# Kernel optimization log

Measured on AMD Instinct MI355X. Metric: run time of the kernel, lower is better.

Reference implementation:

```python
import jax, jax.numpy as jnp
import numpy as np

C_QKV = 1024
C_HIDDEN = 64
NUM_HEADS = 16
INF = 1e9


def setup_inputs() -> dict:
    key = jax.random.key(0)
    ks = jax.random.split(key, 10)
    B, S = 2, 2048
    d = C_QKV
    hd = C_HIDDEN * NUM_HEADS
    sc = 0.02
    return {
        "input_qkv": jax.random.normal(ks[0], (B, S, d), jnp.float32),
        "mask": jnp.ones((B, 1, 1, S), jnp.float32),
        "bias": jax.random.normal(ks[1], (1, NUM_HEADS, S, S), jnp.float32) * sc,
        "wq": jax.random.normal(ks[2], (d, hd), jnp.float32) * sc,
        "wk": jax.random.normal(ks[3], (d, hd), jnp.float32) * sc,
        "wv": jax.random.normal(ks[4], (d, hd), jnp.float32) * sc,
        "wg": jax.random.normal(ks[5], (d, hd), jnp.float32) * sc,
        "bg": jnp.zeros((hd,), jnp.float32),
        "wo": jax.random.normal(ks[6], (hd, d), jnp.float32) * sc,
        "bo": jnp.zeros((d,), jnp.float32),
    }


def reference(input_qkv, mask, bias, wq, wk, wv, wg, bg, wo, bo):
    B, S, _ = input_qkv.shape
    H, C = NUM_HEADS, C_HIDDEN
    # projections -> [B, H, S, C]
    q = (input_qkv @ wq).reshape(B, S, H, C).transpose(0, 2, 1, 3)
    k = (input_qkv @ wk).reshape(B, S, H, C).transpose(0, 2, 1, 3)
    v = (input_qkv @ wv).reshape(B, S, H, C).transpose(0, 2, 1, 3)
    q = q / jnp.asarray(C, q.dtype) ** 0.5
    # scores [B, H, S, S] with additive mask and pair bias
    a = jnp.einsum("bhqc,bhkc->bhqk", q, k)
    a = a + (mask - 1.0) * INF + bias
    a = jax.nn.softmax(a, axis=-1)
    o = jnp.einsum("bhqk,bhkc->bhqc", a, v).transpose(0, 2, 1, 3)  # [B,S,H,C]
    gate = jax.nn.sigmoid(input_qkv @ wg + bg).reshape(B, S, H, C)
    o = (o * gate).reshape(B, S, H * C)
    return o @ wo + bo
```

## Files before the change

### kernel.cpp

```cpp
#include <hip/hip_runtime.h>
#include <hip/hip_bf16.h>
#include <stdint.h>

typedef unsigned short u16;
typedef __attribute__((ext_vector_type(8))) short short8;
typedef __attribute__((ext_vector_type(4))) short short4v;
typedef __attribute__((ext_vector_type(4))) float f32x4;

#define MFMA16 __builtin_amdgcn_mfma_f32_16x16x32_bf16

#define GLOAD_LDS16(gsrc, ldst) \
  __builtin_amdgcn_global_load_lds((const __attribute__((address_space(1))) void*)(gsrc), \
                                   (__attribute__((address_space(3))) void*)(ldst), 16, 0, 0)

__device__ __forceinline__ u16 f2bf(float x) {
  union { float f; uint32_t u; } v; v.f = x;
  uint32_t r = v.u + 0x7FFFu + ((v.u >> 16) & 1u);
  return (u16)(r >> 16);
}
__device__ __forceinline__ u16 f2bf_rn(float x) {
  __hip_bfloat16 h = __float2bfloat16(x);
  return *reinterpret_cast<u16*>(&h);
}
__device__ __forceinline__ float bf2f(u16 b) {
  union { uint32_t u; float f; } v; v.u = ((uint32_t)b) << 16;
  return v.f;
}

__global__ __launch_bounds__(256) void convert_bf16_kernel(
    const float* __restrict__ in, u16* __restrict__ out, int n) {
  int i = (blockIdx.x * 256 + threadIdx.x) * 8;
  if (i >= n) return;
  float4 a = *(const float4*)(in + i);
  float4 b = *(const float4*)(in + i + 4);
  short8 t;
  t[0] = (short)f2bf(a.x); t[1] = (short)f2bf(a.y);
  t[2] = (short)f2bf(a.z); t[3] = (short)f2bf(a.w);
  t[4] = (short)f2bf(b.x); t[5] = (short)f2bf(b.y);
  t[6] = (short)f2bf(b.z); t[7] = (short)f2bf(b.w);
  *(short8*)(out + i) = t;
}

__global__ __launch_bounds__(256) void transpose_w64_4(
    const float* __restrict__ w0, const float* __restrict__ w1,
    const float* __restrict__ w2, const float* __restrict__ w3,
    u16* __restrict__ WT) {
  __shared__ float tile[64][68];
  const int t = threadIdx.x;
  const int z = blockIdx.z;
  const float* W = (z == 0) ? w0 : (z == 1) ? w1 : (z == 2) ? w2 : w3;
  u16* dst_base = WT + (size_t)z * 1024 * 1024;
  const int k0 = blockIdx.x * 64, n0 = blockIdx.y * 64;
  {
    int r = t >> 2, c0 = (t & 3) * 16;
    const float* src = W + (size_t)(k0 + r) * 1024 + n0 + c0;
#pragma unroll
    for (int j = 0; j < 16; j += 4) {
      float4 v = *(const float4*)(src + j);
      tile[r][c0 + j + 0] = v.x; tile[r][c0 + j + 1] = v.y;
      tile[r][c0 + j + 2] = v.z; tile[r][c0 + j + 3] = v.w;
    }
  }
  __syncthreads();
  {
    int n = t >> 2, kq = (t & 3) * 16;
    short8 t0, t1;
#pragma unroll
    for (int j = 0; j < 8; ++j)  t0[j] = (short)f2bf(tile[kq + j][n]);
#pragma unroll
    for (int j = 0; j < 8; ++j)  t1[j] = (short)f2bf(tile[kq + 8 + j][n]);
    u16* dst = dst_base + (size_t)(n0 + n) * 1024 + k0 + kq;
    *(short8*)dst = t0;
    *(short8*)(dst + 8) = t1;
  }
}

__global__ __launch_bounds__(256) void transpose_w64(
    const float* __restrict__ W, u16* __restrict__ WT, int KK, int NN) {
  __shared__ float tile[64][68];
  const int t = threadIdx.x;
  const int k0 = blockIdx.x * 64, n0 = blockIdx.y * 64;
  {
    int r = t >> 2, c0 = (t & 3) * 16;
    const float* src = W + (size_t)(k0 + r) * NN + n0 + c0;
#pragma unroll
    for (int j = 0; j < 16; j += 4) {
      float4 v = *(const float4*)(src + j);
      tile[r][c0 + j + 0] = v.x; tile[r][c0 + j + 1] = v.y;
      tile[r][c0 + j + 2] = v.z; tile[r][c0 + j + 3] = v.w;
    }
  }
  __syncthreads();
  {
    int n = t >> 2, kq = (t & 3) * 16;
    short8 t0, t1;
#pragma unroll
    for (int j = 0; j < 8; ++j)  t0[j] = (short)f2bf(tile[kq + j][n]);
#pragma unroll
    for (int j = 0; j < 8; ++j)  t1[j] = (short)f2bf(tile[kq + 8 + j][n]);
    u16* dst = WT + (size_t)(n0 + n) * KK + k0 + kq;
    *(short8*)dst = t0;
    *(short8*)(dst + 8) = t1;
  }
}

__global__ __launch_bounds__(256) void transpose_v64(
    const u16* __restrict__ vin, u16* __restrict__ vout) {
  __shared__ u16 tile[64][80];
  const int t = threadIdx.x;
  const int s0 = blockIdx.x * 64;
  const int bh = blockIdx.y;
  const int b = bh >> 4, h = bh & 15;
  {
    int r = t >> 2, c0 = (t & 3) * 16;
    const u16* src = vin + (size_t)(b * 2048 + s0 + r) * 1024 + h * 64 + c0;
    *(short8*)&tile[r][c0] = *(const short8*)src;
    *(short8*)&tile[r][c0 + 8] = *(const short8*)(src + 8);
  }
  __syncthreads();
  {
    int c = t >> 2, s4 = (t & 3) * 16;
    short8 t0, t1;
#pragma unroll
    for (int j = 0; j < 8; ++j) t0[j] = (short)tile[s4 + j][c];
#pragma unroll
    for (int j = 0; j < 8; ++j) t1[j] = (short)tile[s4 + 8 + j][c];
    u16* dst = vout + (size_t)(bh * 64 + c) * 2048 + s0 + s4;
    *(short8*)dst = t0;
    *(short8*)(dst + 8) = t1;
  }
}

__global__ __launch_bounds__(256) void gemm_bt128(
    const u16* __restrict__ A, const u16* __restrict__ BTbase,
    void* __restrict__ dstbase, const float* __restrict__ bvec, int mode) {
  const int K = 1024;
  const int tid = threadIdx.x, lane = tid & 63, w = tid >> 6;
  const int wr = w >> 1, wc = w & 1;
  const int l15 = lane & 15, lg = lane >> 4;
  const int z = (mode < 0) ? (int)blockIdx.z : mode;
  const u16* BT = (mode < 0) ? BTbase + (size_t)z * 1024 * 1024 : BTbase;
  const int rbase = blockIdx.x * 128;
  const int nbase = blockIdx.y * 128;
  __shared__ u16 lsA[128 * 64];
  __shared__ u16 lsB[128 * 64];
  f32x4 acc[4][4] = {};
  const int col8 = (lane & 7) * 8;
  for (int kt = 0; kt < K / 64; ++kt) {
#pragma unroll
    for (int i = 0; i < 4; ++i) {
      int row = w * 32 + i * 8 + (lane >> 3);
      const u16* sa = A + (size_t)(rbase + row) * K + kt * 64 + col8;
      GLOAD_LDS16(sa, lsA + (w * 32 + i * 8) * 64 + lane * 8);
      const u16* sb = BT + (size_t)(nbase + row) * K + kt * 64 + col8;
      GLOAD_LDS16(sb, lsB + (w * 32 + i * 8) * 64 + lane * 8);
    }
    __syncthreads();
#pragma unroll
    for (int kk = 0; kk < 2; ++kk) {
      short8 af[4], bfr[4];
#pragma unroll
      for (int m = 0; m < 4; ++m)
        af[m] = *(const short8*)&lsA[(wr * 64 + m * 16 + l15) * 64 + kk * 32 + lg * 8];
#pragma unroll
      for (int n = 0; n < 4; ++n)
        bfr[n] = *(const short8*)&lsB[(wc * 64 + n * 16 + l15) * 64 + kk * 32 + lg * 8];
#pragma unroll
      for (int m = 0; m < 4; ++m)
#pragma unroll
        for (int n = 0; n < 4; ++n)
          acc[m][n] = MFMA16(af[m], bfr[n], acc[m][n], 0, 0, 0);
    }
    __syncthreads();
  }
  const int r0 = rbase + wr * 64;
  const int c0 = nbase + wc * 64;
  if (z == 4) {
    float* out = (float*)dstbase;
#pragma unroll
    for (int m = 0; m < 4; ++m)
#pragma unroll
      for (int n = 0; n < 4; ++n)
#pragma unroll
        for (int i = 0; i < 4; ++i) {
          int r = r0 + m * 16 + lg * 4 + i;
          int c = c0 + n * 16 + l15;
          out[(size_t)r * 1024 + c] = acc[m][n][i] + bvec[c];
        }
  } else {
    u16* dq = (u16*)dstbase + (size_t)z * 4096 * 1024;
#pragma unroll
    for (int m = 0; m < 4; ++m)
#pragma unroll
      for (int n = 0; n < 4; ++n)
#pragma unroll
        for (int i = 0; i < 4; ++i) {
          int r = r0 + m * 16 + lg * 4 + i;
          int c = c0 + n * 16 + l15;
          float v = acc[m][n][i];
          if (z == 0) v *= 0.125f;
          else if (z == 3) v = 1.f / (1.f + __expf(-(v + bvec[c])));
          dq[(size_t)r * 1024 + c] = f2bf(v);
        }
  }
}

__global__ __launch_bounds__(256, 3) void attn_kernel(
    const u16* __restrict__ qws, const u16* __restrict__ kws,
    const u16* __restrict__ vt, const u16* __restrict__ gws,
    const float* __restrict__ bias, const float* __restrict__ mask,
    u16* __restrict__ og) {
  const int tid = threadIdx.x;
  const int lane = tid & 63;
  const int w = tid >> 6;
  const int l15 = lane & 15, lg = lane >> 4;
  const int bx = blockIdx.x;
  const int qt = (bx & 7) | ((bx >> 4) << 3);
  const int b = (bx >> 3) & 1;
  const int h = blockIdx.y;

  __shared__ __align__(16) u16 ring[4][4096];
  __shared__ __align__(16) u16 lsP[4][1280];
  __shared__ __align__(16) u16 lsM[2048];

  const float* bias_base = bias + ((size_t)h * 2048 + qt * 128) * 2048;
  const u16* vt_base = vt + (size_t)((b * 16 + h) * 64) * 2048;
  const u16* k_base = kws + (size_t)(b * 2048) * 1024 + h * 64;

  {
    float4 m0 = *(const float4*)(mask + b * 2048 + tid * 8);
    float4 m1 = *(const float4*)(mask + b * 2048 + tid * 8 + 4);
    short8 mm;
    mm[0] = (short)f2bf((m0.x - 1.f) * 1e9f); mm[1] = (short)f2bf((m0.y - 1.f) * 1e9f);
    mm[2] = (short)f2bf((m0.z - 1.f) * 1e9f); mm[3] = (short)f2bf((m0.w - 1.f) * 1e9f);
    mm[4] = (short)f2bf((m1.x - 1.f) * 1e9f); mm[5] = (short)f2bf((m1.y - 1.f) * 1e9f);
    mm[6] = (short)f2bf((m1.z - 1.f) * 1e9f); mm[7] = (short)f2bf((m1.w - 1.f) * 1e9f);
    *(short8*)&lsM[tid * 8] = mm;
  }

  const size_t qrow0 = (size_t)(b * 2048 + qt * 128 + w * 32 + l15) * 1024 + h * 64;
  const size_t qrow1 = qrow0 + 16 * 1024;
  short8 qf00 = *(const short8*)(qws + qrow0 + lg * 8);
  short8 qf01 = *(const short8*)(qws + qrow0 + 32 + lg * 8);
  short8 qf10 = *(const short8*)(qws + qrow1 + lg * 8);
  short8 qf11 = *(const short8*)(qws + qrow1 + 32 + lg * 8);
  asm volatile("" :: "v"(qf00), "v"(qf01), "v"(qf10), "v"(qf11));
  asm volatile("s_waitcnt vmcnt(0)" ::: "memory");

  f32x4 O[2][4] = {};
  float lacc0 = 0.f, lacc1 = 0.f;
  f32x4 bA0, bA1, bA2, bA3, bB0, bB1, bB2, bB3, bC0, bC1, bC2, bC3;

#define STAGE_KV(SLOT, KW) {                                                        \
    int r_ = tid >> 3, cg_ = tid & 7;                                               \
    GLOAD_LDS16(k_base + (size_t)((KW) * 32 + r_) * 1024 + ((cg_ ^ (r_ & 7)) * 8),  \
                &ring[SLOT][tid * 8]);                                              \
    int c_ = tid >> 2, kg_ = tid & 3;                                               \
    int sw_ = (c_ & 3) ^ ((c_ >> 2) & 3);                                           \
    GLOAD_LDS16(vt_base + (size_t)c_ * 2048 + (KW) * 32 + ((kg_ ^ sw_) * 8),        \
                &ring[SLOT][2048 + tid * 8]); }

#define BIAS_ISSUE(R0, R1, R2, R3, KW) {                                            \
    const float* bp_ = bias_base + (size_t)(w * 32 + l15) * 2048 + (KW) * 32 + lg * 4; \
    asm volatile("global_load_dwordx4 %0, %1, off" : "=v"(R0) : "v"(bp_));          \
    asm volatile("global_load_dwordx4 %0, %1, off" : "=v"(R1) : "v"(bp_ + 16));     \
    asm volatile("global_load_dwordx4 %0, %1, off" : "=v"(R2) : "v"(bp_ + 16 * 2048)); \
    asm volatile("global_load_dwordx4 %0, %1, off" : "=v"(R3) : "v"(bp_ + 16 * 2048 + 16)); \
  }

#define COMPUTE(SLOT, KB, BR00, BR01, BR10, BR11) {                                 \
    const u16* Kc_ = &ring[SLOT][0];                                                \
    const u16* Vc_ = &ring[SLOT][2048];                                             \
    const int sw_ = l15 & 7;                                                        \
    short8 kf0a = *(const short8*)&Kc_[(l15) * 64 + ((lg ^ sw_) * 8)];              \
    short8 kf0b = *(const short8*)&Kc_[(l15) * 64 + (((4 + lg) ^ sw_) * 8)];        \
    short8 kf1a = *(const short8*)&Kc_[(16 + l15) * 64 + ((lg ^ sw_) * 8)];         \
    short8 kf1b = *(const short8*)&Kc_[(16 + l15) * 64 + (((4 + lg) ^ sw_) * 8)];   \
    short4v mk0 = *(const short4v*)&lsM[(KB) * 32 + lg * 4];                        \
    short4v mk1 = *(const short4v*)&lsM[(KB) * 32 + 16 + lg * 4];                   \
    f32x4 ci00, ci01, ci10, ci11;                                                   \
    _Pragma("unroll") for (int i = 0; i < 4; ++i) {                                 \
      float m0_ = bf2f((u16)mk0[i]), m1_ = bf2f((u16)mk1[i]);                       \
      ci00[i] = BR00[i] + m0_; ci01[i] = BR01[i] + m1_;                             \
      ci10[i] = BR10[i] + m0_; ci11[i] = BR11[i] + m1_;                             \
    }                                                                               \
    f32x4 s00 = MFMA16(kf0a, qf00, ci00, 0, 0, 0);                                 \
    s00 = MFMA16(kf0b, qf01, s00, 0, 0, 0);                                         \
    f32x4 s01 = MFMA16(kf1a, qf00, ci01, 0, 0, 0);                                 \
    s01 = MFMA16(kf1b, qf01, s01, 0, 0, 0);                                         \
    f32x4 s10 = MFMA16(kf0a, qf10, ci10, 0, 0, 0);                                 \
    s10 = MFMA16(kf0b, qf11, s10, 0, 0, 0);                                         \
    f32x4 s11 = MFMA16(kf1a, qf10, ci11, 0, 0, 0);                                 \
    s11 = MFMA16(kf1b, qf11, s11, 0, 0, 0);                                         \
    short4v p00, p01, p10, p11;                                                     \
    _Pragma("unroll") for (int i = 0; i < 4; ++i) {                                 \
      float e00 = __expf(s00[i]); lacc0 += e00; p00[i] = (short)f2bf_rn(e00);       \
      float e01 = __expf(s01[i]); lacc0 += e01; p01[i] = (short)f2bf_rn(e01);       \
      float e10 = __expf(s10[i]); lacc1 += e10; p10[i] = (short)f2bf_rn(e10);       \
      float e11 = __expf(s11[i]); lacc1 += e11; p11[i] = (short)f2bf_rn(e11);       \
    }                                                                               \
    *(short4v*)&lsP[w][(l15) * 40 + lg * 4] = p00;                                  \
    *(short4v*)&lsP[w][(l15) * 40 + 16 + lg * 4] = p01;                             \
    *(short4v*)&lsP[w][(16 + l15) * 40 + lg * 4] = p10;                             \
    *(short4v*)&lsP[w][(16 + l15) * 40 + 16 + lg * 4] = p11;                        \
    short8 pf0 = *(const short8*)&lsP[w][(l15) * 40 + lg * 8];                      \
    short8 pf1 = *(const short8*)&lsP[w][(16 + l15) * 40 + lg * 8];                 \
    _Pragma("unroll") for (int cf = 0; cf < 4; ++cf) {                              \
      int c_ = cf * 16 + l15;                                                       \
      short8 vf_ = *(const short8*)&Vc_[c_ * 32 +                                   \
                                        ((lg ^ ((c_ & 3) ^ ((c_ >> 2) & 3))) * 8)]; \
      O[0][cf] = MFMA16(vf_, pf0, O[0][cf], 0, 0, 0);                               \
      O[1][cf] = MFMA16(vf_, pf1, O[1][cf], 0, 0, 0);                               \
    } }

#define BODY(KB, N, X0, X1, X2, X3) {                                               \
    if ((KB) + 3 < 64) STAGE_KV(((KB) + 3) & 3, (KB) + 3);                          \
    COMPUTE((KB) & 3, KB, X0, X1, X2, X3);                                          \
    if ((KB) + 3 < 64) BIAS_ISSUE(X0, X1, X2, X3, (KB) + 3);                        \
    asm volatile("s_waitcnt vmcnt(" #N ")" ::: "memory");                           \
    asm volatile("s_waitcnt lgkmcnt(0)" ::: "memory");                              \
    __builtin_amdgcn_sched_barrier(0);                                              \
    __builtin_amdgcn_s_barrier(); }

  STAGE_KV(0, 0);
  BIAS_ISSUE(bA0, bA1, bA2, bA3, 0);
  STAGE_KV(1, 1);
  BIAS_ISSUE(bB0, bB1, bB2, bB3, 1);
  STAGE_KV(2, 2);
  BIAS_ISSUE(bC0, bC1, bC2, bC3, 2);
  asm volatile("s_waitcnt vmcnt(12)" ::: "memory");
  asm volatile("s_waitcnt lgkmcnt(0)" ::: "memory");
  __builtin_amdgcn_sched_barrier(0);
  __builtin_amdgcn_s_barrier();

  for (int kb3 = 0; kb3 < 60; kb3 += 3) {
    BODY(kb3,     12, bA0, bA1, bA2, bA3);
    BODY(kb3 + 1, 12, bB0, bB1, bB2, bB3);
    BODY(kb3 + 2, 12, bC0, bC1, bC2, bC3);
  }
  BODY(60, 12, bA0, bA1, bA2, bA3);
  BODY(61,  6, bB0, bB1, bB2, bB3);
  BODY(62,  0, bC0, bC1, bC2, bC3);
  BODY(63,  0, bA0, bA1, bA2, bA3);

  lacc0 += __shfl_xor(lacc0, 16); lacc0 += __shfl_xor(lacc0, 32);
  lacc1 += __shfl_xor(lacc1, 16); lacc1 += __shfl_xor(lacc1, 32);
  {
    float inv0 = 1.f / lacc0, inv1 = 1.f / lacc1;
#pragma unroll
    for (int cf = 0; cf < 4; ++cf) {
      short4v ga = *(const short4v*)(gws + qrow0 + cf * 16 + lg * 4);
      short4v gb = *(const short4v*)(gws + qrow1 + cf * 16 + lg * 4);
      short4v oa, ob;
#pragma unroll
      for (int i = 0; i < 4; ++i) {
        oa[i] = (short)f2bf_rn(O[0][cf][i] * inv0 * bf2f((u16)ga[i]));
        ob[i] = (short)f2bf_rn(O[1][cf][i] * inv1 * bf2f((u16)gb[i]));
      }
      *(short4v*)(og + qrow0 + cf * 16 + lg * 4) = oa;
      *(short4v*)(og + qrow1 + cf * 16 + lg * 4) = ob;
    }
  }
#undef STAGE_KV
#undef BIAS_ISSUE
#undef COMPUTE
#undef BODY
}

extern "C" void kernel_launch(void* const* d_in, const int* in_sizes, int n_in,
                              void* d_out, int out_size, void* d_ws, size_t ws_size,
                              hipStream_t stream) {
  const float* x    = (const float*)d_in[0];
  const float* mask = (const float*)d_in[1];
  const float* bias = (const float*)d_in[2];
  const float* wq   = (const float*)d_in[3];
  const float* wk   = (const float*)d_in[4];
  const float* wv   = (const float*)d_in[5];
  const float* wg   = (const float*)d_in[6];
  const float* bg   = (const float*)d_in[7];
  const float* wo   = (const float*)d_in[8];
  const float* bo   = (const float*)d_in[9];
  float* out = (float*)d_out;

  char* ws = (char*)d_ws;
  const size_t MB = 1ull << 20;
  u16* xb   = (u16*)(ws + 0);
  u16* wt   = (u16*)(ws + 8 * MB);
  u16* wot  = (u16*)(ws + 16 * MB);
  u16* proj = (u16*)(ws + 18 * MB);
  u16* vtp  = (u16*)(ws + 50 * MB);
  u16* og   = (u16*)(ws + 58 * MB);
  const size_t PSZ = (size_t)4096 * 1024;

  convert_bf16_kernel<<<2048, 256, 0, stream>>>(x, xb, 4096 * 1024);

  transpose_w64_4<<<dim3(16, 16, 4), 256, 0, stream>>>(wq, wk, wv, wg, wt);
  transpose_w64<<<dim3(16, 16), 256, 0, stream>>>(wo, wot, 1024, 1024);

  gemm_bt128<<<dim3(32, 8, 4), 256, 0, stream>>>(xb, wt, (void*)proj, bg, -1);

  transpose_v64<<<dim3(32, 32), 256, 0, stream>>>(proj + 2 * PSZ, vtp);

  attn_kernel<<<dim3(32, 16), 256, 0, stream>>>(proj, proj + PSZ, vtp, proj + 3 * PSZ,
                                                bias, mask, og);

  gemm_bt128<<<dim3(32, 8, 1), 256, 0, stream>>>(og, wot, (void*)out, bo, 4);
}
```

Baseline: 224.5 us.

## Widen attention key tile to 64 with three-slot ring and fewer barriers

The attention kernel now processes 64 keys per iteration instead of 32. It uses a three-slot K/V ring in LDS, fetches more bias loads per step with a two-step prefetch depth, and switches V to the same XOR swizzle as K. Halving the iteration count cuts the per-step barrier and waitcnt overhead and gives the MFMAs more work between syncs. In exchange, register and LDS use grow, launch bounds drop to 2 blocks per CU, and prefetch depth shrinks from three tiles to two.

```diff
diff --git a/kernel.cpp b/kernel.cpp
--- a/kernel.cpp
+++ b/kernel.cpp
@@ -205,7 +205,7 @@
   }
 }
 
-__global__ __launch_bounds__(256, 3) void attn_kernel(
+__global__ __launch_bounds__(256, 2) void attn_kernel(
     const u16* __restrict__ qws, const u16* __restrict__ kws,
     const u16* __restrict__ vt, const u16* __restrict__ gws,
     const float* __restrict__ bias, const float* __restrict__ mask,
@@ -219,8 +219,8 @@
   const int b = (bx >> 3) & 1;
   const int h = blockIdx.y;
 
-  __shared__ __align__(16) u16 ring[4][4096];
-  __shared__ __align__(16) u16 lsP[4][1280];
+  __shared__ __align__(16) u16 ring[3][8192];
+  __shared__ __align__(16) u16 lsP[4][2304];
   __shared__ __align__(16) u16 lsM[2048];
 
   const float* bias_base = bias + ((size_t)h * 2048 + qt * 128) * 2048;
@@ -249,99 +249,102 @@
 
   f32x4 O[2][4] = {};
   float lacc0 = 0.f, lacc1 = 0.f;
-  f32x4 bA0, bA1, bA2, bA3, bB0, bB1, bB2, bB3, bC0, bC1, bC2, bC3;
+  f32x4 bA0, bA1, bA2, bA3, bA4, bA5, bA6, bA7;
+  f32x4 bB0, bB1, bB2, bB3, bB4, bB5, bB6, bB7;
 
 #define STAGE_KV(SLOT, KW) {                                                        \
-    int r_ = tid >> 3, cg_ = tid & 7;                                               \
-    GLOAD_LDS16(k_base + (size_t)((KW) * 32 + r_) * 1024 + ((cg_ ^ (r_ & 7)) * 8),  \
-                &ring[SLOT][tid * 8]);                                              \
-    int c_ = tid >> 2, kg_ = tid & 3;                                               \
-    int sw_ = (c_ & 3) ^ ((c_ >> 2) & 3);                                           \
-    GLOAD_LDS16(vt_base + (size_t)c_ * 2048 + (KW) * 32 + ((kg_ ^ sw_) * 8),        \
-                &ring[SLOT][2048 + tid * 8]); }
-
-#define BIAS_ISSUE(R0, R1, R2, R3, KW) {                                            \
-    const float* bp_ = bias_base + (size_t)(w * 32 + l15) * 2048 + (KW) * 32 + lg * 4; \
+    _Pragma("unroll") for (int it = 0; it < 2; ++it) {                              \
+      int g_ = it * 256 + tid;                                                      \
+      int r_ = g_ >> 3, cg_ = g_ & 7;                                               \
+      GLOAD_LDS16(k_base + (size_t)((KW) * 64 + r_) * 1024 + ((cg_ ^ (r_ & 7)) * 8),\
+                  &ring[SLOT][g_ * 8]);                                             \
+      GLOAD_LDS16(vt_base + (size_t)r_ * 2048 + (KW) * 64 + ((cg_ ^ (r_ & 7)) * 8), \
+                  &ring[SLOT][4096 + g_ * 8]);                                      \
+    } }
+
+#define BIAS_ISSUE(R0, R1, R2, R3, R4, R5, R6, R7, KW) {                            \
+    const float* bp_ = bias_base + (size_t)(w * 32 + l15) * 2048 + (KW) * 64 + lg * 4; \
     asm volatile("global_load_dwordx4 %0, %1, off" : "=v"(R0) : "v"(bp_));          \
     asm volatile("global_load_dwordx4 %0, %1, off" : "=v"(R1) : "v"(bp_ + 16));     \
-    asm volatile("global_load_dwordx4 %0, %1, off" : "=v"(R2) : "v"(bp_ + 16 * 2048)); \
-    asm volatile("global_load_dwordx4 %0, %1, off" : "=v"(R3) : "v"(bp_ + 16 * 2048 + 16)); \
-  }
-
-#define COMPUTE(SLOT, KB, BR00, BR01, BR10, BR11) {                                 \
+    asm volatile("global_load_dwordx4 %0, %1, off" : "=v"(R2) : "v"(bp_ + 32));     \
+    asm volatile("global_load_dwordx4 %0, %1, off" : "=v"(R3) : "v"(bp_ + 48));     \
+    asm volatile("global_load_dwordx4 %0, %1, off" : "=v"(R4) : "v"(bp_ + 16 * 2048)); \
+    asm volatile("global_load_dwordx4 %0, %1, off" : "=v"(R5) : "v"(bp_ + 16 * 2048 + 16)); \
+    asm volatile("global_load_dwordx4 %0, %1, off" : "=v"(R6) : "v"(bp_ + 16 * 2048 + 32)); \
+    asm volatile("global_load_dwordx4 %0, %1, off" : "=v"(R7) : "v"(bp_ + 16 * 2048 + 48)); \
+  }
+
+#define COMPUTE(SLOT, KB, X0, X1, X2, X3, X4, X5, X6, X7) {                         \
     const u16* Kc_ = &ring[SLOT][0];                                                \
-    const u16* Vc_ = &ring[SLOT][2048];                                             \
-    const int sw_ = l15 & 7;                                                        \
-    short8 kf0a = *(const short8*)&Kc_[(l15) * 64 + ((lg ^ sw_) * 8)];              \
-    short8 kf0b = *(const short8*)&Kc_[(l15) * 64 + (((4 + lg) ^ sw_) * 8)];        \
-    short8 kf1a = *(const short8*)&Kc_[(16 + l15) * 64 + ((lg ^ sw_) * 8)];         \
-    short8 kf1b = *(const short8*)&Kc_[(16 + l15) * 64 + (((4 + lg) ^ sw_) * 8)];   \
-    short4v mk0 = *(const short4v*)&lsM[(KB) * 32 + lg * 4];                        \
-    short4v mk1 = *(const short4v*)&lsM[(KB) * 32 + 16 + lg * 4];                   \
-    f32x4 ci00, ci01, ci10, ci11;                                                   \
-    _Pragma("unroll") for (int i = 0; i < 4; ++i) {                                 \
-      float m0_ = bf2f((u16)mk0[i]), m1_ = bf2f((u16)mk1[i]);                       \
-      ci00[i] = BR00[i] + m0_; ci01[i] = BR01[i] + m1_;                             \
-      ci10[i] = BR10[i] + m0_; ci11[i] = BR11[i] + m1_;                             \
+    const u16* Vc_ = &ring[SLOT][4096];                                             \
+    f32x4 bb0[4] = {X0, X1, X2, X3};                                                \
+    f32x4 bb1[4] = {X4, X5, X6, X7};                                                \
+    f32x4 s_[2][4];                                                                 \
+    _Pragma("unroll") for (int kt = 0; kt < 4; ++kt) {                              \
+      int krow_ = kt * 16 + l15;                                                    \
+      int sw_ = krow_ & 7;                                                          \
+      short8 kfa_ = *(const short8*)&Kc_[(krow_ * 8 + (lg ^ sw_)) * 8];             \
+      short8 kfb_ = *(const short8*)&Kc_[(krow_ * 8 + ((4 + lg) ^ sw_)) * 8];       \
+      short4v mk_ = *(const short4v*)&lsM[(KB) * 64 + kt * 16 + lg * 4];            \
+      f32x4 ci0_, ci1_;                                                             \
+      _Pragma("unroll") for (int i = 0; i < 4; ++i) {                               \
+        float m_ = bf2f((u16)mk_[i]);                                               \
+        ci0_[i] = bb0[kt][i] + m_;                                                  \
+        ci1_[i] = bb1[kt][i] + m_;                                                  \
+      }                                                                             \
+      s_[0][kt] = MFMA16(kfa_, qf00, ci0_, 0, 0, 0);                                \
+      s_[0][kt] = MFMA16(kfb_, qf01, s_[0][kt], 0, 0, 0);                           \
+      s_[1][kt] = MFMA16(kfa_, qf10, ci1_, 0, 0, 0);                                \
+      s_[1][kt] = MFMA16(kfb_, qf11, s_[1][kt], 0, 0, 0);                           \
     }                                                                               \
-    f32x4 s00 = MFMA16(kf0a, qf00, ci00, 0, 0, 0);                                 \
-    s00 = MFMA16(kf0b, qf01, s00, 0, 0, 0);                                         \
-    f32x4 s01 = MFMA16(kf1a, qf00, ci01, 0, 0, 0);                                 \
-    s01 = MFMA16(kf1b, qf01, s01, 0, 0, 0);                                         \
-    f32x4 s10 = MFMA16(kf0a, qf10, ci10, 0, 0, 0);                                 \
-    s10 = MFMA16(kf0b, qf11, s10, 0, 0, 0);                                         \
-    f32x4 s11 = MFMA16(kf1a, qf10, ci11, 0, 0, 0);                                 \
-    s11 = MFMA16(kf1b, qf11, s11, 0, 0, 0);                                         \
-    short4v p00, p01, p10, p11;                                                     \
-    _Pragma("unroll") for (int i = 0; i < 4; ++i) {                                 \
-      float e00 = __expf(s00[i]); lacc0 += e00; p00[i] = (short)f2bf_rn(e00);       \
-      float e01 = __expf(s01[i]); lacc0 += e01; p01[i] = (short)f2bf_rn(e01);       \
-      float e10 = __expf(s10[i]); lacc1 += e10; p10[i] = (short)f2bf_rn(e10);       \
-      float e11 = __expf(s11[i]); lacc1 += e11; p11[i] = (short)f2bf_rn(e11);       \
+    _Pragma("unroll") for (int kt = 0; kt < 4; ++kt) {                              \
+      short4v p0_, p1_;                                                             \
+      _Pragma("unroll") for (int i = 0; i < 4; ++i) {                               \
+        float e0_ = __expf(s_[0][kt][i]); lacc0 += e0_; p0_[i] = (short)f2bf_rn(e0_); \
+        float e1_ = __expf(s_[1][kt][i]); lacc1 += e1_; p1_[i] = (short)f2bf_rn(e1_); \
+      }                                                                             \
+      *(short4v*)&lsP[w][(l15) * 72 + kt * 16 + lg * 4] = p0_;                      \
+      *(short4v*)&lsP[w][(16 + l15) * 72 + kt * 16 + lg * 4] = p1_;                 \
     }                                                                               \
-    *(short4v*)&lsP[w][(l15) * 40 + lg * 4] = p00;                                  \
-    *(short4v*)&lsP[w][(l15) * 40 + 16 + lg * 4] = p01;                             \
-    *(short4v*)&lsP[w][(16 + l15) * 40 + lg * 4] = p10;                             \
-    *(short4v*)&lsP[w][(16 + l15) * 40 + 16 + lg * 4] = p11;                        \
-    short8 pf0 = *(const short8*)&lsP[w][(l15) * 40 + lg * 8];                      \
-    short8 pf1 = *(const short8*)&lsP[w][(16 + l15) * 40 + lg * 8];                 \
+    short8 pf00_ = *(const short8*)&lsP[w][(l15) * 72 + lg * 8];                    \
+    short8 pf01_ = *(const short8*)&lsP[w][(l15) * 72 + 32 + lg * 8];               \
+    short8 pf10_ = *(const short8*)&lsP[w][(16 + l15) * 72 + lg * 8];               \
+    short8 pf11_ = *(const short8*)&lsP[w][(16 + l15) * 72 + 32 + lg * 8];          \
     _Pragma("unroll") for (int cf = 0; cf < 4; ++cf) {                              \
       int c_ = cf * 16 + l15;                                                       \
-      short8 vf_ = *(const short8*)&Vc_[c_ * 32 +                                   \
-                                        ((lg ^ ((c_ & 3) ^ ((c_ >> 2) & 3))) * 8)]; \
-      O[0][cf] = MFMA16(vf_, pf0, O[0][cf], 0, 0, 0);                               \
-      O[1][cf] = MFMA16(vf_, pf1, O[1][cf], 0, 0, 0);                               \
+      int sw_ = c_ & 7;                                                             \
+      short8 vf0_ = *(const short8*)&Vc_[(c_ * 8 + (lg ^ sw_)) * 8];                \
+      short8 vf1_ = *(const short8*)&Vc_[(c_ * 8 + ((4 + lg) ^ sw_)) * 8];          \
+      O[0][cf] = MFMA16(vf0_, pf00_, O[0][cf], 0, 0, 0);                            \
+      O[0][cf] = MFMA16(vf1_, pf01_, O[0][cf], 0, 0, 0);                            \
+      O[1][cf] = MFMA16(vf0_, pf10_, O[1][cf], 0, 0, 0);                            \
+      O[1][cf] = MFMA16(vf1_, pf11_, O[1][cf], 0, 0, 0);                            \
     } }
 
-#define BODY(KB, N, X0, X1, X2, X3) {                                               \
-    if ((KB) + 3 < 64) STAGE_KV(((KB) + 3) & 3, (KB) + 3);                          \
-    COMPUTE((KB) & 3, KB, X0, X1, X2, X3);                                          \
-    if ((KB) + 3 < 64) BIAS_ISSUE(X0, X1, X2, X3, (KB) + 3);                        \
+#define BODY(KB, N, X0, X1, X2, X3, X4, X5, X6, X7) {                               \
+    if ((KB) + 2 < 32) STAGE_KV(((KB) + 2) % 3, (KB) + 2);                          \
+    COMPUTE((KB) % 3, KB, X0, X1, X2, X3, X4, X5, X6, X7);                          \
+    if ((KB) + 2 < 32) BIAS_ISSUE(X0, X1, X2, X3, X4, X5, X6, X7, (KB) + 2);        \
     asm volatile("s_waitcnt vmcnt(" #N ")" ::: "memory");                           \
     asm volatile("s_waitcnt lgkmcnt(0)" ::: "memory");                              \
     __builtin_amdgcn_sched_barrier(0);                                              \
     __builtin_amdgcn_s_barrier(); }
 
   STAGE_KV(0, 0);
-  BIAS_ISSUE(bA0, bA1, bA2, bA3, 0);
+  BIAS_ISSUE(bA0, bA1, bA2, bA3, bA4, bA5, bA6, bA7, 0);
   STAGE_KV(1, 1);
-  BIAS_ISSUE(bB0, bB1, bB2, bB3, 1);
-  STAGE_KV(2, 2);
-  BIAS_ISSUE(bC0, bC1, bC2, bC3, 2);
+  BIAS_ISSUE(bB0, bB1, bB2, bB3, bB4, bB5, bB6, bB7, 1);
   asm volatile("s_waitcnt vmcnt(12)" ::: "memory");
   asm volatile("s_waitcnt lgkmcnt(0)" ::: "memory");
   __builtin_amdgcn_sched_barrier(0);
   __builtin_amdgcn_s_barrier();
 
-  for (int kb3 = 0; kb3 < 60; kb3 += 3) {
-    BODY(kb3,     12, bA0, bA1, bA2, bA3);
-    BODY(kb3 + 1, 12, bB0, bB1, bB2, bB3);
-    BODY(kb3 + 2, 12, bC0, bC1, bC2, bC3);
-  }
-  BODY(60, 12, bA0, bA1, bA2, bA3);
-  BODY(61,  6, bB0, bB1, bB2, bB3);
-  BODY(62,  0, bC0, bC1, bC2, bC3);
-  BODY(63,  0, bA0, bA1, bA2, bA3);
+  for (int kb2 = 0; kb2 < 30; kb2 += 2) {
+    BODY(kb2,     12, bA0, bA1, bA2, bA3, bA4, bA5, bA6, bA7);
+    BODY(kb2 + 1, 12, bB0, bB1, bB2, bB3, bB4, bB5, bB6, bB7);
+  }
+  BODY(30, 0, bA0, bA1, bA2, bA3, bA4, bA5, bA6, bA7);
+  BODY(31, 0, bB0, bB1, bB2, bB3, bB4, bB5, bB6, bB7);
 
   lacc0 += __shfl_xor(lacc0, 16); lacc0 += __shfl_xor(lacc0, 32);
   lacc1 += __shfl_xor(lacc1, 16); lacc1 += __shfl_xor(lacc1, 32);
```

Measured after the change: 218.0 us. -2.9%, faster.
